# Kernel optimization log

Hardware: AMD Instinct MI355X
Metric: run time of the kernel (lower is better)

## Reference

```python
import jax, jax.numpy as jnp
import numpy as np

N, NFEAT, NHID, NCLASS, NHEADS = 4096, 256, 16, 16, 8
ALPHA = 0.2
NEG_INF = -9e15


def setup_inputs() -> dict:
    key = jax.random.key(0)
    ks = jax.random.split(key, 8)
    x = jax.random.normal(ks[0], (N, NFEAT), dtype=jnp.float32)
    adj = (jax.random.uniform(ks[1], (N, N)) < 0.01).astype(jnp.float32)
    adj = jnp.maximum(adj, jnp.eye(N, dtype=jnp.float32))
    # per-head weights for the NHEADS concat layers
    W = jax.random.normal(ks[2], (NHEADS, NFEAT, NHID), dtype=jnp.float32) * 0.1
    a_src = jax.random.normal(ks[3], (NHEADS, NHID), dtype=jnp.float32) * 0.1
    a_dst = jax.random.normal(ks[4], (NHEADS, NHID), dtype=jnp.float32) * 0.1
    # output attention layer (concat=False)
    W_out = jax.random.normal(ks[5], (NHEADS * NHID, NCLASS), dtype=jnp.float32) * 0.1
    a_out_src = jax.random.normal(ks[6], (NCLASS,), dtype=jnp.float32) * 0.1
    a_out_dst = jax.random.normal(ks[7], (NCLASS,), dtype=jnp.float32) * 0.1
    return {"x": x, "adj": adj, "W": W, "a_src": a_src, "a_dst": a_dst,
            "W_out": W_out, "a_out_src": a_out_src, "a_out_dst": a_out_dst}


def _gat_layer(h, adj_mask, W, a_s, a_d, concat):
    # h: [N,F]; W: [H,F,D] (or [F,D] for single head treated as H=1)
    Wh = jnp.einsum('nf,hfd->hnd', h, W)              # [H,N,D]
    src = jnp.einsum('hnd,hd->hn', Wh, a_s)           # [H,N]
    dst = jnp.einsum('hnd,hd->hn', Wh, a_d)           # [H,N]
    e = jax.nn.leaky_relu(src[:, :, None] + dst[:, None, :], ALPHA)  # [H,N,N]
    e = jnp.where(adj_mask > 0, e, NEG_INF)
    att = jax.nn.softmax(e, axis=-1)                  # masked softmax over neighbors
    out = jnp.einsum('hnm,hmd->hnd', att, Wh)         # [H,N,D]
    if concat:
        out = jax.nn.elu(out)
    return out


def reference(x, adj, W, a_src, a_dst, W_out, a_out_src, a_out_dst):
    # multi-head concat layers (dropout in eval mode -> identity)
    h = _gat_layer(x, adj, W, a_src, a_dst, concat=True)          # [H,N,D]
    h = jnp.transpose(h, (1, 0, 2)).reshape(N, NHEADS * NHID)     # concat heads
    # output attention layer (single head, concat=False), then outer ELU
    out = _gat_layer(h, adj, W_out[None], a_out_src[None], a_out_dst[None], concat=False)
    return jax.nn.elu(out[0])                                     # [N, NCLASS]
```

## Files before the change

### kernel.cpp

```cpp
#include <hip/hip_runtime.h>

#define NN 4096
#define NFEAT 256
#define NHID 16
#define NHEADS 8
#define NCOL 128
#define NCLASS 16
#define MAXN 256
#define LALPHA 0.2f
#define BNODES 16
#define XPAD 20
#define EPAD 260

__global__ __launch_bounds__(256) void prep_kernel(
    const float* __restrict__ adj, const float* __restrict__ x,
    const float* __restrict__ W, const float* __restrict__ a_src,
    const float* __restrict__ a_dst,
    int* __restrict__ nbr, int* __restrict__ cnt,
    float* __restrict__ Wh1, float* __restrict__ src1, float* __restrict__ dst1) {
  __shared__ float xT[NFEAT * XPAD];
  __shared__ int scnt;
  int t = threadIdx.x;

  if (blockIdx.x < NN) {
    int row = blockIdx.x;
    const float4* arow = reinterpret_cast<const float4*>(adj + (size_t)row * NN);
    if (t == 0) scnt = 0;
    __syncthreads();
    int* rn = nbr + (size_t)row * MAXN;
    int lane = t & 63;
    unsigned long long below = lane ? (~0ULL >> (64 - lane)) : 0ULL;
#pragma unroll
    for (int it = 0; it < NN / 4 / 256; ++it) {
      int q = t + it * 256;
      float4 v = arow[q];
      int base = q * 4;
      unsigned long long m0 = __ballot(v.x > 0.f);
      unsigned long long m1 = __ballot(v.y > 0.f);
      unsigned long long m2 = __ballot(v.z > 0.f);
      unsigned long long m3 = __ballot(v.w > 0.f);
      int c0 = __popcll(m0), c1 = __popcll(m1), c2 = __popcll(m2), c3 = __popcll(m3);
      int tot = c0 + c1 + c2 + c3;
      int wbase = 0;
      if (lane == 0 && tot) wbase = atomicAdd(&scnt, tot);
      wbase = __shfl(wbase, 0);
      if (v.x > 0.f) { int p = wbase + __popcll(m0 & below);           if (p < MAXN) rn[p] = base;     }
      if (v.y > 0.f) { int p = wbase + c0 + __popcll(m1 & below);      if (p < MAXN) rn[p] = base + 1; }
      if (v.z > 0.f) { int p = wbase + c0 + c1 + __popcll(m2 & below); if (p < MAXN) rn[p] = base + 2; }
      if (v.w > 0.f) { int p = wbase + c0 + c1 + c2 + __popcll(m3 & below); if (p < MAXN) rn[p] = base + 3; }
    }
    __syncthreads();
    if (t == 0) cnt[row] = scnt < MAXN ? scnt : MAXN;
  } else {
    int bn = (blockIdx.x - NN) * BNODES;
#pragma unroll
    for (int it = 0; it < BNODES; ++it) {
      xT[t * XPAD + it] = x[(size_t)(bn + it) * NFEAT + t];
    }
    __syncthreads();
    int cg = t & 31, ng = t >> 5;
    const float* Wp = W + (cg >> 2) * (NFEAT * NHID) + ((cg & 3) << 2);
    float acc[2][4] = {};
#pragma unroll 4
    for (int f = 0; f < NFEAT; ++f) {
      float4 wv = *reinterpret_cast<const float4*>(Wp + f * NHID);
      float2 xv = *reinterpret_cast<const float2*>(&xT[f * XPAD + ng * 2]);
      acc[0][0] += xv.x * wv.x; acc[0][1] += xv.x * wv.y;
      acc[0][2] += xv.x * wv.z; acc[0][3] += xv.x * wv.w;
      acc[1][0] += xv.y * wv.x; acc[1][1] += xv.y * wv.y;
      acc[1][2] += xv.y * wv.z; acc[1][3] += xv.y * wv.w;
    }
    int col0 = cg * 4;
    float4 as4 = *reinterpret_cast<const float4*>(a_src + col0);
    float4 ad4 = *reinterpret_cast<const float4*>(a_dst + col0);
#pragma unroll
    for (int i = 0; i < 2; ++i) {
      int n = bn + ng * 2 + i;
      *reinterpret_cast<float4*>(Wh1 + (size_t)n * NCOL + col0) =
          make_float4(acc[i][0], acc[i][1], acc[i][2], acc[i][3]);
      float vs = acc[i][0] * as4.x + acc[i][1] * as4.y + acc[i][2] * as4.z + acc[i][3] * as4.w;
      float vd = acc[i][0] * ad4.x + acc[i][1] * ad4.y + acc[i][2] * ad4.z + acc[i][3] * ad4.w;
      vs += __shfl_xor(vs, 1); vs += __shfl_xor(vs, 2);
      vd += __shfl_xor(vd, 1); vd += __shfl_xor(vd, 2);
      if ((cg & 3) == 0) {
        src1[n * NHEADS + (cg >> 2)] = vs;
        dst1[n * NHEADS + (cg >> 2)] = vd;
      }
    }
  }
}

__global__ __launch_bounds__(128) void layer1_agg_kernel(
    const int* __restrict__ nbr, const int* __restrict__ cnt,
    const float* __restrict__ Wh1, const float* __restrict__ src1,
    const float* __restrict__ dst1, const float* __restrict__ Wout,
    const float* __restrict__ a2s, const float* __restrict__ a2d,
    float* __restrict__ Wh2, float* __restrict__ src2, float* __restrict__ dst2) {
  int n = blockIdx.x, t = threadIdx.x;
  int h = t >> 4, l = t & 15;
  int c = cnt[n];
  __shared__ int snb[MAXN];
  __shared__ float e[NHEADS * EPAD];
  __shared__ float hs[NCOL];
  __shared__ float part[NHEADS][NCLASS];
  for (int j = t; j < c; j += 128) snb[j] = nbr[(size_t)n * MAXN + j];
  __syncthreads();
  for (int idx = t; idx < c * NHEADS; idx += 128) {
    int j = idx >> 3, hh = idx & 7;
    float ee = src1[n * NHEADS + hh] + dst1[snb[j] * NHEADS + hh];
    e[hh * EPAD + j] = ee > 0.f ? ee : LALPHA * ee;
  }
  __syncthreads();
  float m = -1e30f;
  for (int j = l; j < c; j += 16) m = fmaxf(m, e[h * EPAD + j]);
  m = fmaxf(m, __shfl_xor(m, 8)); m = fmaxf(m, __shfl_xor(m, 4));
  m = fmaxf(m, __shfl_xor(m, 2)); m = fmaxf(m, __shfl_xor(m, 1));
  float s = 0.f;
  for (int j = l; j < c; j += 16) {
    float w = __expf(e[h * EPAD + j] - m);
    e[h * EPAD + j] = w;
    s += w;
  }
  s += __shfl_xor(s, 8); s += __shfl_xor(s, 4);
  s += __shfl_xor(s, 2); s += __shfl_xor(s, 1);
  float rs = 1.f / s;
  __syncthreads();
  float acc = 0.f;
#pragma unroll 4
  for (int j = 0; j < c; ++j)
    acc += e[h * EPAD + j] * Wh1[(size_t)snb[j] * NCOL + t];
  acc *= rs;
  hs[t] = acc > 0.f ? acc : (__expf(acc) - 1.f);
  __syncthreads();
  int cc = t & 15, kg = t >> 4;
  float p = 0.f;
#pragma unroll
  for (int k = 0; k < 16; ++k)
    p += hs[kg * 16 + k] * Wout[(kg * 16 + k) * NCLASS + cc];
  part[kg][cc] = p;
  __syncthreads();
  if (t < NCLASS) {
    float a = 0.f;
#pragma unroll
    for (int kg2 = 0; kg2 < NHEADS; ++kg2) a += part[kg2][t];
    Wh2[n * NCLASS + t] = a;
    float vs = a * a2s[t], vd = a * a2d[t];
#pragma unroll
    for (int off = 8; off >= 1; off >>= 1) {
      vs += __shfl_xor(vs, off);
      vd += __shfl_xor(vd, off);
    }
    if (t == 0) { src2[n] = vs; dst2[n] = vd; }
  }
}

__global__ __launch_bounds__(256) void layer2_agg_kernel(
    const int* __restrict__ nbr, const int* __restrict__ cnt,
    const float* __restrict__ Wh2, const float* __restrict__ src2,
    const float* __restrict__ dst2, float* __restrict__ out) {
  int g = threadIdx.x >> 4, d = threadIdx.x & 15;
  int n = blockIdx.x * 16 + g;
  int c = cnt[n];
  const int* nb = nbr + (size_t)n * MAXN;
  float si = src2[n];
  float m = -1e30f;
#pragma unroll 4
  for (int j = 0; j < c; ++j) {
    float ee = si + dst2[nb[j]];
    ee = ee > 0.f ? ee : LALPHA * ee;
    m = fmaxf(m, ee);
  }
  float s = 0.f, acc = 0.f;
#pragma unroll 2
  for (int j = 0; j < c; ++j) {
    int jj = nb[j];
    float ee = si + dst2[jj];
    ee = ee > 0.f ? ee : LALPHA * ee;
    float w = __expf(ee - m);
    s += w;
    acc += w * Wh2[jj * NCLASS + d];
  }
  acc /= s;
  out[n * NCLASS + d] = acc > 0.f ? acc : (__expf(acc) - 1.f);
}

extern "C" void kernel_launch(void* const* d_in, const int* in_sizes, int n_in,
                              void* d_out, int out_size, void* d_ws, size_t ws_size,
                              hipStream_t stream) {
  const float* x     = (const float*)d_in[0];
  const float* adj   = (const float*)d_in[1];
  const float* W     = (const float*)d_in[2];
  const float* a_src = (const float*)d_in[3];
  const float* a_dst = (const float*)d_in[4];
  const float* W_out = (const float*)d_in[5];
  const float* a_os  = (const float*)d_in[6];
  const float* a_od  = (const float*)d_in[7];
  float* out = (float*)d_out;

  char* ws = (char*)d_ws;
  size_t off = 0;
  auto alloc = [&](size_t bytes) -> void* {
    void* p = ws + off;
    off += (bytes + 255) & ~(size_t)255;
    return p;
  };
  int*   nbr  = (int*)alloc((size_t)NN * MAXN * sizeof(int));
  int*   cnt  = (int*)alloc((size_t)NN * sizeof(int));
  float* Wh1  = (float*)alloc((size_t)NN * NCOL * sizeof(float));
  float* src1 = (float*)alloc((size_t)NN * NHEADS * sizeof(float));
  float* dst1 = (float*)alloc((size_t)NN * NHEADS * sizeof(float));
  float* Wh2  = (float*)alloc((size_t)NN * NCLASS * sizeof(float));
  float* src2 = (float*)alloc((size_t)NN * sizeof(float));
  float* dst2 = (float*)alloc((size_t)NN * sizeof(float));

  hipLaunchKernelGGL(prep_kernel, dim3(NN + NN / BNODES), dim3(256), 0, stream,
                     adj, x, W, a_src, a_dst, nbr, cnt, Wh1, src1, dst1);
  hipLaunchKernelGGL(layer1_agg_kernel, dim3(NN), dim3(128), 0, stream,
                     nbr, cnt, Wh1, src1, dst1, W_out, a_os, a_od, Wh2, src2, dst2);
  hipLaunchKernelGGL(layer2_agg_kernel, dim3(NN / 16), dim3(256), 0, stream,
                     nbr, cnt, Wh2, src2, dst2, out);
}
```

Baseline: 165.5 us.

## Split adjacency scan into quarter-row blocks and parallelize layer-2 neighbor loop

```diff
diff --git a/kernel.cpp b/kernel.cpp
--- a/kernel.cpp
+++ b/kernel.cpp
@@ -9,6 +9,7 @@
 #define MAXN 256
 #define LALPHA 0.2f
 #define BNODES 16
+#define NPROJ (NN / BNODES)
 #define XPAD 20
 #define EPAD 260
 
@@ -19,40 +20,33 @@
     int* __restrict__ nbr, int* __restrict__ cnt,
     float* __restrict__ Wh1, float* __restrict__ src1, float* __restrict__ dst1) {
   __shared__ float xT[NFEAT * XPAD];
-  __shared__ int scnt;
   int t = threadIdx.x;
 
-  if (blockIdx.x < NN) {
-    int row = blockIdx.x;
-    const float4* arow = reinterpret_cast<const float4*>(adj + (size_t)row * NN);
-    if (t == 0) scnt = 0;
-    __syncthreads();
-    int* rn = nbr + (size_t)row * MAXN;
+  if (blockIdx.x >= NPROJ) {
+    int bid = blockIdx.x - NPROJ;
+    int row = bid >> 2, quarter = bid & 3;
+    const float4* arow =
+        reinterpret_cast<const float4*>(adj + (size_t)row * NN) + quarter * 256;
+    float4 v = arow[t];
     int lane = t & 63;
     unsigned long long below = lane ? (~0ULL >> (64 - lane)) : 0ULL;
-#pragma unroll
-    for (int it = 0; it < NN / 4 / 256; ++it) {
-      int q = t + it * 256;
-      float4 v = arow[q];
-      int base = q * 4;
-      unsigned long long m0 = __ballot(v.x > 0.f);
-      unsigned long long m1 = __ballot(v.y > 0.f);
-      unsigned long long m2 = __ballot(v.z > 0.f);
-      unsigned long long m3 = __ballot(v.w > 0.f);
-      int c0 = __popcll(m0), c1 = __popcll(m1), c2 = __popcll(m2), c3 = __popcll(m3);
-      int tot = c0 + c1 + c2 + c3;
-      int wbase = 0;
-      if (lane == 0 && tot) wbase = atomicAdd(&scnt, tot);
-      wbase = __shfl(wbase, 0);
-      if (v.x > 0.f) { int p = wbase + __popcll(m0 & below);           if (p < MAXN) rn[p] = base;     }
-      if (v.y > 0.f) { int p = wbase + c0 + __popcll(m1 & below);      if (p < MAXN) rn[p] = base + 1; }
-      if (v.z > 0.f) { int p = wbase + c0 + c1 + __popcll(m2 & below); if (p < MAXN) rn[p] = base + 2; }
-      if (v.w > 0.f) { int p = wbase + c0 + c1 + c2 + __popcll(m3 & below); if (p < MAXN) rn[p] = base + 3; }
-    }
-    __syncthreads();
-    if (t == 0) cnt[row] = scnt < MAXN ? scnt : MAXN;
+    unsigned long long m0 = __ballot(v.x > 0.f);
+    unsigned long long m1 = __ballot(v.y > 0.f);
+    unsigned long long m2 = __ballot(v.z > 0.f);
+    unsigned long long m3 = __ballot(v.w > 0.f);
+    int c0 = __popcll(m0), c1 = __popcll(m1), c2 = __popcll(m2), c3 = __popcll(m3);
+    int tot = c0 + c1 + c2 + c3;
+    int wbase = 0;
+    if (lane == 0 && tot) wbase = atomicAdd(&cnt[row], tot);
+    wbase = __shfl(wbase, 0);
+    int* rn = nbr + (size_t)row * MAXN;
+    int base = quarter * 1024 + t * 4;
+    if (v.x > 0.f) { int p = wbase + __popcll(m0 & below);                if (p < MAXN) rn[p] = base;     }
+    if (v.y > 0.f) { int p = wbase + c0 + __popcll(m1 & below);           if (p < MAXN) rn[p] = base + 1; }
+    if (v.z > 0.f) { int p = wbase + c0 + c1 + __popcll(m2 & below);      if (p < MAXN) rn[p] = base + 2; }
+    if (v.w > 0.f) { int p = wbase + c0 + c1 + c2 + __popcll(m3 & below); if (p < MAXN) rn[p] = base + 3; }
   } else {
-    int bn = (blockIdx.x - NN) * BNODES;
+    int bn = blockIdx.x * BNODES;
 #pragma unroll
     for (int it = 0; it < BNODES; ++it) {
       xT[t * XPAD + it] = x[(size_t)(bn + it) * NFEAT + t];
@@ -98,7 +92,7 @@
     float* __restrict__ Wh2, float* __restrict__ src2, float* __restrict__ dst2) {
   int n = blockIdx.x, t = threadIdx.x;
   int h = t >> 4, l = t & 15;
-  int c = cnt[n];
+  int c = cnt[n]; c = c < MAXN ? c : MAXN;
   __shared__ int snb[MAXN];
   __shared__ float e[NHEADS * EPAD];
   __shared__ float hs[NCOL];
@@ -126,7 +120,7 @@
   float rs = 1.f / s;
   __syncthreads();
   float acc = 0.f;
-#pragma unroll 4
+#pragma unroll 8
   for (int j = 0; j < c; ++j)
     acc += e[h * EPAD + j] * Wh1[(size_t)snb[j] * NCOL + t];
   acc *= rs;
@@ -158,21 +152,23 @@
     const int* __restrict__ nbr, const int* __restrict__ cnt,
     const float* __restrict__ Wh2, const float* __restrict__ src2,
     const float* __restrict__ dst2, float* __restrict__ out) {
-  int g = threadIdx.x >> 4, d = threadIdx.x & 15;
-  int n = blockIdx.x * 16 + g;
-  int c = cnt[n];
+  int wave = threadIdx.x >> 6;
+  int lane = threadIdx.x & 63;
+  int d = lane & 15, g = lane >> 4;
+  int n = blockIdx.x * 4 + wave;
+  int c = cnt[n]; c = c < MAXN ? c : MAXN;
   const int* nb = nbr + (size_t)n * MAXN;
   float si = src2[n];
   float m = -1e30f;
-#pragma unroll 4
-  for (int j = 0; j < c; ++j) {
+  for (int j = g; j < c; j += 4) {
     float ee = si + dst2[nb[j]];
     ee = ee > 0.f ? ee : LALPHA * ee;
     m = fmaxf(m, ee);
   }
+  m = fmaxf(m, __shfl_xor(m, 16));
+  m = fmaxf(m, __shfl_xor(m, 32));
   float s = 0.f, acc = 0.f;
-#pragma unroll 2
-  for (int j = 0; j < c; ++j) {
+  for (int j = g; j < c; j += 4) {
     int jj = nb[j];
     float ee = si + dst2[jj];
     ee = ee > 0.f ? ee : LALPHA * ee;
@@ -180,8 +176,12 @@
     s += w;
     acc += w * Wh2[jj * NCLASS + d];
   }
-  acc /= s;
-  out[n * NCLASS + d] = acc > 0.f ? acc : (__expf(acc) - 1.f);
+  s += __shfl_xor(s, 16); s += __shfl_xor(s, 32);
+  acc += __shfl_xor(acc, 16); acc += __shfl_xor(acc, 32);
+  if (g == 0) {
+    acc /= s;
+    out[n * NCLASS + d] = acc > 0.f ? acc : (__expf(acc) - 1.f);
+  }
 }
 
 extern "C" void kernel_launch(void* const* d_in, const int* in_sizes, int n_in,
@@ -213,10 +213,11 @@
   float* src2 = (float*)alloc((size_t)NN * sizeof(float));
   float* dst2 = (float*)alloc((size_t)NN * sizeof(float));
 
-  hipLaunchKernelGGL(prep_kernel, dim3(NN + NN / BNODES), dim3(256), 0, stream,
+  hipMemsetAsync(cnt, 0, NN * sizeof(int), stream);
+  hipLaunchKernelGGL(prep_kernel, dim3(NPROJ + 4 * NN), dim3(256), 0, stream,
                      adj, x, W, a_src, a_dst, nbr, cnt, Wh1, src1, dst1);
   hipLaunchKernelGGL(layer1_agg_kernel, dim3(NN), dim3(128), 0, stream,
                      nbr, cnt, Wh1, src1, dst1, W_out, a_os, a_od, Wh2, src2, dst2);
-  hipLaunchKernelGGL(layer2_agg_kernel, dim3(NN / 16), dim3(256), 0, stream,
+  hipLaunchKernelGGL(layer2_agg_kernel, dim3(NN / 4), dim3(256), 0, stream,
                      nbr, cnt, Wh2, src2, dst2, out);
 }
```

After: 161.4 us. -2.5%, faster.
